# Kernel tuning notes

Hardware: AMD Instinct MI355X
Metric: run time of the kernel (lower is better)

Reference implementation:

```python
import jax, jax.numpy as jnp
import numpy as np

HIDDEN = 2048
NUM_Q_HEADS = 16
NUM_KV_HEADS = 4
HEAD_DIM = HIDDEN // NUM_Q_HEADS  # 128
KV_REP = NUM_Q_HEADS // NUM_KV_HEADS  # 4
KV_DIM = HEAD_DIM * NUM_KV_HEADS


def setup_inputs() -> dict:
    key = jax.random.key(0)
    ks = jax.random.split(key, 9)
    B, S = 2, 2048
    s_in = 1.0 / np.sqrt(HIDDEN)
    return {
        "hidden_states": jax.random.normal(ks[0], (B, S, HIDDEN), dtype=jnp.float32),
        "Wq": jax.random.normal(ks[1], (HIDDEN, HIDDEN), dtype=jnp.float32) * s_in,
        "bq": jnp.zeros((HIDDEN,), dtype=jnp.float32),
        "Wk": jax.random.normal(ks[2], (HIDDEN, KV_DIM), dtype=jnp.float32) * s_in,
        "bk": jnp.zeros((KV_DIM,), dtype=jnp.float32),
        "Wv": jax.random.normal(ks[3], (HIDDEN, KV_DIM), dtype=jnp.float32) * s_in,
        "bv": jnp.zeros((KV_DIM,), dtype=jnp.float32),
        "Wo": jax.random.normal(ks[4], (HIDDEN, HIDDEN), dtype=jnp.float32) * s_in,
        "bo": jnp.zeros((HIDDEN,), dtype=jnp.float32),
    }


def reference(hidden_states, Wq, bq, Wk, bk, Wv, bv, Wo, bo):
    B, S, H = hidden_states.shape
    # projections
    q = hidden_states @ Wq + bq  # [B,S,H]
    k = hidden_states @ Wk + bk  # [B,S,KV_DIM]
    v = hidden_states @ Wv + bv  # [B,S,KV_DIM]
    # [B, heads, S, head_dim]
    q = q.reshape(B, S, NUM_Q_HEADS, HEAD_DIM).transpose(0, 2, 1, 3)
    k = k.reshape(B, S, NUM_KV_HEADS, HEAD_DIM).transpose(0, 2, 1, 3)
    v = v.reshape(B, S, NUM_KV_HEADS, HEAD_DIM).transpose(0, 2, 1, 3)
    # repeat_interleave KV heads to match q heads
    k = jnp.repeat(k, KV_REP, axis=1)  # [B,Hq,S,hd]
    v = jnp.repeat(v, KV_REP, axis=1)
    scale = 1.0 / np.sqrt(HEAD_DIM)
    scores = jnp.einsum('bhqd,bhkd->bhqk', q, k) * scale  # [B,Hq,S,S]
    causal = jnp.triu(jnp.ones((S, S), dtype=bool), k=1)
    scores = jnp.where(causal[None, None], -jnp.inf, scores)
    probs = jax.nn.softmax(scores, axis=-1)
    ctx = jnp.einsum('bhqk,bhkd->bhqd', probs, v)  # [B,Hq,S,hd]
    ctx = ctx.transpose(0, 2, 1, 3).reshape(B, S, H)
    return ctx @ Wo + bo
```

## Files before the change

kernel.cpp:

```cpp
#include <hip/hip_runtime.h>
#include <hip/hip_bf16.h>
#include <stdint.h>

#define SEQ 2048
#define BATCH 2
#define NTOK (SEQ * BATCH)
#define HID 2048
#define NQH 16
#define NKVH 4
#define HD 128
#define KVD 512

typedef __bf16 bf16x8 __attribute__((ext_vector_type(8)));
typedef float f32x4 __attribute__((ext_vector_type(4)));
typedef float f32x16 __attribute__((ext_vector_type(16)));
typedef unsigned int u32;

__device__ __forceinline__ unsigned short f2bf(float f) {
    uint32_t u = __builtin_bit_cast(uint32_t, f);
    uint32_t r = (u + 0x7fffu + ((u >> 16) & 1u)) >> 16;
    return (unsigned short)r;
}

__device__ __forceinline__ u32 cvtpk(float lo, float hi) {
    u32 r;
    asm("v_cvt_pk_bf16_f32 %0, %1, %2" : "=v"(r) : "v"(lo), "v"(hi));
    return r;
}

__device__ __forceinline__ void gload16(const void* g, void* l) {
    __builtin_amdgcn_global_load_lds((const __attribute__((address_space(1))) u32*)g,
                                     (__attribute__((address_space(3))) u32*)l, 16, 0, 0);
}

__global__ void cvt_f32_bf16(const float* __restrict__ in, unsigned short* __restrict__ out, int n4) {
    int i = blockIdx.x * blockDim.x + threadIdx.x;
    int stride = gridDim.x * blockDim.x;
    for (; i < n4; i += stride) {
        float4 v = ((const float4*)in)[i];
        ushort4 o;
        o.x = f2bf(v.x); o.y = f2bf(v.y); o.z = f2bf(v.z); o.w = f2bf(v.w);
        ((ushort4*)out)[i] = o;
    }
}

__global__ __launch_bounds__(256) void transpose_all(const float* __restrict__ Wq,
                                                     const float* __restrict__ Wk,
                                                     const float* __restrict__ Wv,
                                                     const float* __restrict__ Wo,
                                                     unsigned short* __restrict__ Wqkvt,
                                                     unsigned short* __restrict__ Wot) {
    __shared__ unsigned short tile[64][72];
    const int y = blockIdx.y;
    const float* W;
    unsigned short* dst;
    int N, ny;
    if (y < 32)      { W = Wq; dst = Wqkvt;                        N = 2048; ny = y; }
    else if (y < 40) { W = Wk; dst = Wqkvt + (size_t)2048 * HID;   N = 512;  ny = y - 32; }
    else if (y < 48) { W = Wv; dst = Wqkvt + (size_t)2560 * HID;   N = 512;  ny = y - 40; }
    else             { W = Wo; dst = Wot;                          N = 2048; ny = y - 48; }
    const int k0 = blockIdx.x * 64, n0 = ny * 64;
    const int t = threadIdx.x;
    const int r = t >> 4;
    const int c4 = (t & 15) * 4;
    #pragma unroll
    for (int i = 0; i < 4; i++) {
        int row = r + i * 16;
        float4 v = *(const float4*)&W[(size_t)(k0 + row) * N + n0 + c4];
        tile[row][c4 + 0] = f2bf(v.x);
        tile[row][c4 + 1] = f2bf(v.y);
        tile[row][c4 + 2] = f2bf(v.z);
        tile[row][c4 + 3] = f2bf(v.w);
    }
    __syncthreads();
    #pragma unroll
    for (int i = 0; i < 4; i++) {
        int nrow = r + i * 16;
        ushort4 o;
        o.x = tile[c4 + 0][nrow];
        o.y = tile[c4 + 1][nrow];
        o.z = tile[c4 + 2][nrow];
        o.w = tile[c4 + 3][nrow];
        *(ushort4*)&dst[(size_t)(n0 + nrow) * HID + k0 + c4] = o;
    }
}

template <int MODE>
__global__ __launch_bounds__(256) void gemm128(const unsigned short* __restrict__ A,
                                               const unsigned short* __restrict__ Bt,
                                               const float* __restrict__ b0,
                                               const float* __restrict__ b1,
                                               const float* __restrict__ b2,
                                               void* __restrict__ o0,
                                               void* __restrict__ o1,
                                               void* __restrict__ o2) {
    __shared__ unsigned short Asm[2][128 * 64];
    __shared__ unsigned short Bsm[2][128 * 64];
    const int m0 = blockIdx.x * 128;
    const int n0 = blockIdx.y * 128;
    const int t = threadIdx.x;
    const int lane = t & 63, w = t >> 6;
    const int wr = (w >> 1) * 64, wc = (w & 1) * 64;
    const int l16 = lane & 15, lg = lane >> 4;

    f32x4 acc[4][4] = {};

    auto stage = [&](int buf, int kt) {
        const int k0 = kt * 64;
        #pragma unroll
        for (int it = 0; it < 4; it++) {
            int base = it * 256 + w * 64;
            int qc = base + lane;
            int row = qc >> 3, c = qc & 7;
            int col = ((c ^ (row & 7)) << 3);
            gload16(&A[(size_t)(m0 + row) * HID + k0 + col], (char*)&Asm[buf][0] + base * 16);
            gload16(&Bt[(size_t)(n0 + row) * HID + k0 + col], (char*)&Bsm[buf][0] + base * 16);
        }
    };

    stage(0, 0);
    __syncthreads();
    int buf = 0;
    for (int kt = 0; kt < HID / 64; kt++) {
        if (kt < HID / 64 - 1) stage(buf ^ 1, kt + 1);
        const char* Ab = (const char*)&Asm[buf][0];
        const char* Bb = (const char*)&Bsm[buf][0];
        #pragma unroll
        for (int kk = 0; kk < 2; kk++) {
            bf16x8 af[4], bfr[4];
            #pragma unroll
            for (int m = 0; m < 4; m++) {
                int row = wr + m * 16 + l16;
                af[m] = *(const bf16x8*)(Ab + row * 128 + (((kk * 4 + lg) ^ (row & 7)) << 4));
            }
            #pragma unroll
            for (int n = 0; n < 4; n++) {
                int row = wc + n * 16 + l16;
                bfr[n] = *(const bf16x8*)(Bb + row * 128 + (((kk * 4 + lg) ^ (row & 7)) << 4));
            }
            #pragma unroll
            for (int m = 0; m < 4; m++)
                #pragma unroll
                for (int n = 0; n < 4; n++)
                    acc[m][n] = __builtin_amdgcn_mfma_f32_16x16x32_bf16(af[m], bfr[n], acc[m][n], 0, 0, 0);
        }
        __syncthreads();
        buf ^= 1;
    }
    const float sc = 0.08838834764831845f;
    #pragma unroll
    for (int m = 0; m < 4; m++) {
        int row = m0 + wr + m * 16 + lg * 4;
        #pragma unroll
        for (int n = 0; n < 4; n++) {
            int col = n0 + wc + n * 16 + l16;
            #pragma unroll
            for (int r = 0; r < 4; r++) {
                float v = acc[m][n][r];
                int rr = row + r;
                if constexpr (MODE == 0) {
                    if (col < 2048) {
                        v = (v + b0[col]) * sc;
                        ((unsigned short*)o0)[(size_t)rr * HID + col] = f2bf(v);
                    } else if (col < 2560) {
                        int c = col - 2048;
                        v += b1[c];
                        ((unsigned short*)o1)[(size_t)rr * KVD + c] = f2bf(v);
                    } else {
                        int c = col - 2560;
                        v += b2[c];
                        int b = rr >> 11, s = rr & (SEQ - 1);
                        ((unsigned short*)o2)[((size_t)b * KVD + c) * SEQ + s] = f2bf(v);
                    }
                } else {
                    v += b0[col];
                    ((float*)o0)[(size_t)rr * HID + col] = v;
                }
            }
        }
    }
}

__global__ __launch_bounds__(256, 2) void attn(const unsigned short* __restrict__ Q,
                                               const unsigned short* __restrict__ K,
                                               const unsigned short* __restrict__ Vt,
                                               unsigned short* __restrict__ ctx) {
    __shared__ unsigned short Ksm[2][64 * 128];
    __shared__ unsigned short Vsm[2][128 * 64];
    const int n = blockIdx.x;
    const int qt = 15 - (n >> 5);
    const int bh = n & 31;
    const int b = bh >> 4, h = bh & 15, hk = h >> 2;
    const int t = threadIdx.x, w = t >> 6, lane = t & 63;
    const int lam = lane & 31, hi = lane >> 5;
    const int qw = qt * 128 + w * 32;
    const int qg = qw + lam;
    const size_t qrowbase = (size_t)b * SEQ + qw;

    const unsigned short* Kg = K + (size_t)b * SEQ * KVD + hk * HD;
    const unsigned short* Vg = Vt + ((size_t)b * KVD + hk * HD) * SEQ;

    bf16x8 qf[8];
    #pragma unroll
    for (int kc = 0; kc < 8; kc++)
        qf[kc] = *(const bf16x8*)&Q[(qrowbase + lam) * HID + h * HD + kc * 16 + hi * 8];

    f32x16 oacc[4] = {};
    float m = -1e30f, l = 0.f;

    auto stage = [&](int buf, int kt) {
        const int kvb = kt * 64;
        #pragma unroll
        for (int it = 0; it < 4; it++) {
            int base = it * 256 + w * 64;
            int qc = base + lane;
            {
                int row = qc >> 4, c = qc & 15;
                gload16(&Kg[(size_t)(kvb + row) * KVD + ((c ^ (row & 7)) << 3)],
                        (char*)&Ksm[buf][0] + base * 16);
            }
            {
                int row = qc >> 3, c = qc & 7;
                gload16(&Vg[(size_t)row * SEQ + kvb + ((c ^ (row & 7)) << 3)],
                        (char*)&Vsm[buf][0] + base * 16);
            }
        }
    };

    const int ntile = 2 * qt + 2;
    stage(0, 0);
    __syncthreads();
    int buf = 0;
    for (int kt = 0; kt < ntile; kt++) {
        const int kvb = kt * 64;
        if (kt + 1 < ntile) stage(buf ^ 1, kt + 1);
        if (kvb <= qw + 31) {
            const char* Kb = (const char*)&Ksm[buf][0];
            const char* Vb = (const char*)&Vsm[buf][0];
            f32x16 st0 = {}, st1 = {};
            #pragma unroll
            for (int kc = 0; kc < 8; kc++) {
                int coff = (kc * 32 + hi * 16) ^ ((lam & 7) << 4);
                bf16x8 kf0 = *(const bf16x8*)(Kb + lam * 256 + coff);
                bf16x8 kf1 = *(const bf16x8*)(Kb + (32 + lam) * 256 + coff);
                st0 = __builtin_amdgcn_mfma_f32_32x32x16_bf16(kf0, qf[kc], st0, 0, 0, 0);
                st1 = __builtin_amdgcn_mfma_f32_32x32x16_bf16(kf1, qf[kc], st1, 0, 0, 0);
            }
            if (kvb + 63 > qw) {
                #pragma unroll
                for (int r = 0; r < 16; r++) {
                    int krow = (r & 3) + 8 * (r >> 2) + 4 * hi;
                    if (kvb + krow > qg) st0[r] = -1e30f;
                    if (kvb + 32 + krow > qg) st1[r] = -1e30f;
                }
            }
            float tmax = st0[0];
            #pragma unroll
            for (int r = 1; r < 16; r++) tmax = fmaxf(tmax, st0[r]);
            #pragma unroll
            for (int r = 0; r < 16; r++) tmax = fmaxf(tmax, st1[r]);
            tmax = fmaxf(tmax, __shfl_xor(tmax, 32));
            float mn = fmaxf(m, tmax);
            float sf = __expf(m - mn);
            m = mn;
            float rs = 0.f;
            #pragma unroll
            for (int r = 0; r < 16; r++) { st0[r] = __expf(st0[r] - mn); rs += st0[r]; }
            #pragma unroll
            for (int r = 0; r < 16; r++) { st1[r] = __expf(st1[r] - mn); rs += st1[r]; }
            rs += __shfl_xor(rs, 32);
            l = l * sf + rs;
            #pragma unroll
            for (int dc = 0; dc < 4; dc++)
                #pragma unroll
                for (int r = 0; r < 16; r++) oacc[dc][r] *= sf;
            u32 pw0[4][2], pw1[4][2];
            #pragma unroll
            for (int g = 0; g < 4; g++) {
                pw0[g][0] = cvtpk(st0[4 * g], st0[4 * g + 1]);
                pw0[g][1] = cvtpk(st0[4 * g + 2], st0[4 * g + 3]);
                pw1[g][0] = cvtpk(st1[4 * g], st1[4 * g + 1]);
                pw1[g][1] = cvtpk(st1[4 * g + 2], st1[4 * g + 3]);
            }
            #pragma unroll
            for (int kc = 0; kc < 4; kc++) {
                const u32 (*pw)[2] = (kc >> 1) ? pw1 : pw0;
                int g0 = (kc & 1) * 2;
                u32 own0 = hi ? pw[g0 + 1][0] : pw[g0][0];
                u32 own1 = hi ? pw[g0 + 1][1] : pw[g0][1];
                u32 off0 = hi ? pw[g0][0] : pw[g0 + 1][0];
                u32 off1 = hi ? pw[g0][1] : pw[g0 + 1][1];
                u32 xw0 = __shfl_xor(off0, 32);
                u32 xw1 = __shfl_xor(off1, 32);
                int4 paw;
                paw.x = hi ? xw0 : own0;
                paw.y = hi ? xw1 : own1;
                paw.z = hi ? own0 : xw0;
                paw.w = hi ? own1 : xw1;
                bf16x8 pa = __builtin_bit_cast(bf16x8, paw);
                #pragma unroll
                for (int dc = 0; dc < 4; dc++) {
                    bf16x8 vf = *(const bf16x8*)(Vb + (dc * 32 + lam) * 128 +
                                                 ((kc * 32 + hi * 16) ^ ((lam & 7) << 4)));
                    oacc[dc] = __builtin_amdgcn_mfma_f32_32x32x16_bf16(vf, pa, oacc[dc], 0, 0, 0);
                }
            }
        }
        __syncthreads();
        buf ^= 1;
    }

    float inv = 1.f / l;
    char* osm = (char*)&Ksm[0][0] + w * 8192;
    #pragma unroll
    for (int dc = 0; dc < 4; dc++)
        #pragma unroll
        for (int r = 0; r < 16; r += 2) {
            int d = dc * 32 + (r & 3) + 8 * (r >> 2) + 4 * hi;
            u32 wd = cvtpk(oacc[dc][r] * inv, oacc[dc][r + 1] * inv);
            *(u32*)(osm + lam * 256 + ((d * 2) ^ ((lam & 7) << 4))) = wd;
        }
    __syncthreads();
    const int q2 = lane >> 1, half = lane & 1;
    #pragma unroll
    for (int cc = 0; cc < 8; cc++) {
        bf16x8 v = *(const bf16x8*)(osm + q2 * 256 + (((half * 8 + cc) * 16) ^ ((q2 & 7) << 4)));
        *(bf16x8*)&ctx[(qrowbase + q2) * HID + h * HD + half * 64 + cc * 8] = v;
    }
}

extern "C" void kernel_launch(void* const* d_in, const int* in_sizes, int n_in,
                              void* d_out, int out_size, void* d_ws, size_t ws_size,
                              hipStream_t stream) {
    const float* X  = (const float*)d_in[0];
    const float* Wq = (const float*)d_in[1];
    const float* bq = (const float*)d_in[2];
    const float* Wk = (const float*)d_in[3];
    const float* bk = (const float*)d_in[4];
    const float* Wv = (const float*)d_in[5];
    const float* bv = (const float*)d_in[6];
    const float* Wo = (const float*)d_in[7];
    const float* bo = (const float*)d_in[8];
    float* out = (float*)d_out;

    const size_t MB = 1u << 20;
    char* ws = (char*)d_ws;
    if (ws_size < 76 * MB) return;
    unsigned short* Xb    = (unsigned short*)(ws + 0 * MB);
    unsigned short* Wqkvt = (unsigned short*)(ws + 16 * MB);
    unsigned short* Wot   = (unsigned short*)(ws + 28 * MB);
    unsigned short* Qb    = (unsigned short*)(ws + 36 * MB);
    unsigned short* Kb    = (unsigned short*)(ws + 52 * MB);
    unsigned short* Vtb   = (unsigned short*)(ws + 56 * MB);
    unsigned short* Ctx   = (unsigned short*)(ws + 60 * MB);

    cvt_f32_bf16<<<2048, 256, 0, stream>>>(X, Xb, NTOK * HID / 4);
    transpose_all<<<dim3(32, 80), 256, 0, stream>>>(Wq, Wk, Wv, Wo, Wqkvt, Wot);

    gemm128<0><<<dim3(32, 24), 256, 0, stream>>>(Xb, Wqkvt, bq, bk, bv, Qb, Kb, Vtb);

    attn<<<dim3(512), 256, 0, stream>>>(Qb, Kb, Vtb, Ctx);

    gemm128<1><<<dim3(32, 16), 256, 0, stream>>>(Ctx, Wot, bo, nullptr, nullptr, (void*)out, nullptr, nullptr);
}
```

Before: 227.4 us.

## Replace QKV projection GEMM with 256x256-tile, 8-wave pipelined kernel

Adds a dedicated QKV GEMM that uses 256x256 output tiles with 512 threads, 128KB of LDS split into K-halves, and a fine-grained pipeline of half-tile staging interleaved with MFMA phases. It uses explicit barriers, waitcnt and setprio, plus a block-index swizzle for L2 reuse. The aim is more data reuse per LDS load and better overlap of global loads with matrix math. The output GEMM is kept as a 128-tile kernel specialised to fp32 output. Costs are higher register and LDS pressure, only 192 blocks, and fragile hand-managed synchronisation.

```diff
diff --git a/kernel.cpp b/kernel.cpp
--- a/kernel.cpp
+++ b/kernel.cpp
@@ -32,6 +32,11 @@
     __builtin_amdgcn_global_load_lds((const __attribute__((address_space(1))) u32*)g,
                                      (__attribute__((address_space(3))) u32*)l, 16, 0, 0);
 }
+
+#define BARRIER()  asm volatile("s_barrier" ::: "memory")
+#define LGKM0()    do { asm volatile("s_waitcnt lgkmcnt(0)" ::: "memory"); \
+                        __builtin_amdgcn_sched_barrier(0); } while (0)
+#define VMCNT(n)   asm volatile("s_waitcnt vmcnt(" #n ")" ::: "memory")
 
 __global__ void cvt_f32_bf16(const float* __restrict__ in, unsigned short* __restrict__ out, int n4) {
     int i = blockIdx.x * blockDim.x + threadIdx.x;
@@ -85,15 +90,135 @@
     }
 }
 
-template <int MODE>
-__global__ __launch_bounds__(256) void gemm128(const unsigned short* __restrict__ A,
-                                               const unsigned short* __restrict__ Bt,
-                                               const float* __restrict__ b0,
-                                               const float* __restrict__ b1,
-                                               const float* __restrict__ b2,
-                                               void* __restrict__ o0,
-                                               void* __restrict__ o1,
-                                               void* __restrict__ o2) {
+__global__ __launch_bounds__(512, 2) void gemm_qkv(const unsigned short* __restrict__ A,
+                                                   const unsigned short* __restrict__ Bt,
+                                                   const float* __restrict__ bq,
+                                                   const float* __restrict__ bk,
+                                                   const float* __restrict__ bv,
+                                                   unsigned short* __restrict__ Qo,
+                                                   unsigned short* __restrict__ Ko,
+                                                   unsigned short* __restrict__ Vo) {
+    __shared__ __align__(16) char LDSRAW[131072];
+    const int NTT = HID / 64;
+    const int bid = blockIdx.x;
+    const int swz = (bid % 8) * 24 + bid / 8;
+    const int m0 = (swz % 16) * 256;
+    const int nb = swz / 16;
+    const int n0 = nb * 256;
+    const int tid = threadIdx.x;
+    const int lane = tid & 63, w = tid >> 6;
+    const int wm = w >> 2, wn = w & 3;
+    const int l16 = lane & 15, lg = lane >> 4;
+
+    f32x4 acc[2][4][4] = {};
+
+    auto stageHalf = [&](int ts, int mtx, int kh) {
+        if (ts >= NTT) return;
+        const unsigned short* src = mtx ? (Bt + (size_t)n0 * HID) : (A + (size_t)m0 * HID);
+        const int region = mtx * 65536 + (ts & 1) * 32768 + kh * 16384;
+        #pragma unroll
+        for (int j = 0; j < 2; j++) {
+            int c = j * 512 + tid;
+            int row = c >> 2, s = c & 3;
+            int cg = s ^ ((row >> 1) & 3);
+            gload16(&src[(size_t)row * HID + ts * 64 + kh * 32 + cg * 8],
+                    LDSRAW + region + (j * 512 + w * 64) * 16);
+        }
+    };
+    auto ldsA = [&](int buf, int kh, int mq, bf16x8 (&dst)[4]) {
+        #pragma unroll
+        for (int mf = 0; mf < 4; mf++) {
+            int row = wm * 128 + mq * 64 + mf * 16 + l16;
+            int slot = lg ^ ((row >> 1) & 3);
+            dst[mf] = *(const bf16x8*)(LDSRAW + buf * 32768 + kh * 16384 + row * 64 + slot * 16);
+        }
+    };
+    auto ldsB = [&](int buf, int kh, bf16x8 (&dst)[4]) {
+        #pragma unroll
+        for (int nf = 0; nf < 4; nf++) {
+            int row = wn * 64 + nf * 16 + l16;
+            int slot = lg ^ ((row >> 1) & 3);
+            dst[nf] = *(const bf16x8*)(LDSRAW + 65536 + buf * 32768 + kh * 16384 + row * 64 + slot * 16);
+        }
+    };
+    auto mfma16 = [&](f32x4 (&ac)[4][4], bf16x8 (&a4)[4], bf16x8 (&b4)[4]) {
+        __builtin_amdgcn_s_setprio(1);
+        #pragma unroll
+        for (int mf = 0; mf < 4; mf++)
+            #pragma unroll
+            for (int nf = 0; nf < 4; nf++)
+                ac[mf][nf] = __builtin_amdgcn_mfma_f32_16x16x32_bf16(a4[mf], b4[nf], ac[mf][nf], 0, 0, 0);
+        __builtin_amdgcn_s_setprio(0);
+    };
+
+    stageHalf(0, 0, 0); stageHalf(0, 1, 0); stageHalf(0, 0, 1); stageHalf(0, 1, 1);
+    stageHalf(1, 0, 0); stageHalf(1, 1, 0);
+    VMCNT(4);
+    BARRIER();
+
+    for (int t = 0; t < NTT; t++) {
+        const int buf = t & 1;
+        bf16x8 a4[4], b4[4];
+        ldsA(buf, 0, 0, a4); ldsB(buf, 0, b4);
+        stageHalf(t + 1, 0, 1);
+        BARRIER(); LGKM0();
+        mfma16(acc[0], a4, b4);
+        BARRIER();
+        ldsA(buf, 0, 1, a4);
+        stageHalf(t + 1, 1, 1);
+        BARRIER(); LGKM0();
+        mfma16(acc[1], a4, b4);
+        BARRIER();
+        ldsA(buf, 1, 0, a4); ldsB(buf, 1, b4);
+        stageHalf(t + 2, 0, 0);
+        if (t == NTT - 1) { VMCNT(0); }
+        BARRIER(); LGKM0();
+        mfma16(acc[0], a4, b4);
+        BARRIER();
+        ldsA(buf, 1, 1, a4);
+        stageHalf(t + 2, 1, 0);
+        if (t < NTT - 1) { VMCNT(4); }
+        BARRIER(); LGKM0();
+        mfma16(acc[1], a4, b4);
+        BARRIER();
+    }
+
+    const float sc = 0.08838834764831845f;
+    #pragma unroll
+    for (int mq = 0; mq < 2; mq++) {
+        #pragma unroll
+        for (int mf = 0; mf < 4; mf++) {
+            int row = m0 + wm * 128 + mq * 64 + mf * 16 + lg * 4;
+            #pragma unroll
+            for (int nf = 0; nf < 4; nf++) {
+                int col = n0 + wn * 64 + nf * 16 + l16;
+                #pragma unroll
+                for (int r = 0; r < 4; r++) {
+                    float v = acc[mq][mf][nf][r];
+                    int rr = row + r;
+                    if (nb < 8) {
+                        v = (v + bq[col]) * sc;
+                        Qo[(size_t)rr * HID + col] = f2bf(v);
+                    } else if (nb < 10) {
+                        int c = col - 2048;
+                        v += bk[c];
+                        Ko[(size_t)rr * KVD + c] = f2bf(v);
+                    } else {
+                        int c = col - 2560;
+                        v += bv[c];
+                        int b = rr >> 11, s = rr & (SEQ - 1);
+                        Vo[((size_t)b * KVD + c) * SEQ + s] = f2bf(v);
+                    }
+                }
+            }
+        }
+    }
+}
+
+__global__ __launch_bounds__(256) void gemm_o(const unsigned short* __restrict__ A,
+                                              const unsigned short* __restrict__ Bt,
+                                              const float* __restrict__ bias,
+                                              float* __restrict__ out1) {
     __shared__ unsigned short Asm[2][128 * 64];
     __shared__ unsigned short Bsm[2][128 * 64];
     const int m0 = blockIdx.x * 128;
@@ -147,7 +272,6 @@
         __syncthreads();
         buf ^= 1;
     }
-    const float sc = 0.08838834764831845f;
     #pragma unroll
     for (int m = 0; m < 4; m++) {
         int row = m0 + wr + m * 16 + lg * 4;
@@ -155,28 +279,8 @@
         for (int n = 0; n < 4; n++) {
             int col = n0 + wc + n * 16 + l16;
             #pragma unroll
-            for (int r = 0; r < 4; r++) {
-                float v = acc[m][n][r];
-                int rr = row + r;
-                if constexpr (MODE == 0) {
-                    if (col < 2048) {
-                        v = (v + b0[col]) * sc;
-                        ((unsigned short*)o0)[(size_t)rr * HID + col] = f2bf(v);
-                    } else if (col < 2560) {
-                        int c = col - 2048;
-                        v += b1[c];
-                        ((unsigned short*)o1)[(size_t)rr * KVD + c] = f2bf(v);
-                    } else {
-                        int c = col - 2560;
-                        v += b2[c];
-                        int b = rr >> 11, s = rr & (SEQ - 1);
-                        ((unsigned short*)o2)[((size_t)b * KVD + c) * SEQ + s] = f2bf(v);
-                    }
-                } else {
-                    v += b0[col];
-                    ((float*)o0)[(size_t)rr * HID + col] = v;
-                }
-            }
+            for (int r = 0; r < 4; r++)
+                out1[(size_t)(row + r) * HID + col] = acc[m][n][r] + bias[col];
         }
     }
 }
@@ -357,9 +461,9 @@
     cvt_f32_bf16<<<2048, 256, 0, stream>>>(X, Xb, NTOK * HID / 4);
     transpose_all<<<dim3(32, 80), 256, 0, stream>>>(Wq, Wk, Wv, Wo, Wqkvt, Wot);
 
-    gemm128<0><<<dim3(32, 24), 256, 0, stream>>>(Xb, Wqkvt, bq, bk, bv, Qb, Kb, Vtb);
+    gemm_qkv<<<dim3(192), 512, 0, stream>>>(Xb, Wqkvt, bq, bk, bv, Qb, Kb, Vtb);
 
     attn<<<dim3(512), 256, 0, stream>>>(Qb, Kb, Vtb, Ctx);
 
-    gemm128<1><<<dim3(32, 16), 256, 0, stream>>>(Ctx, Wot, bo, nullptr, nullptr, (void*)out, nullptr, nullptr);
-}
+    gemm_o<<<dim3(32, 16), 256, 0, stream>>>(Ctx, Wot, bo, out);
+}
```

New measurement: 222.0 us. 1.02x faster.
